# Optimization experiments

Measured on AMD Instinct MI355X. Metric: run time of the kernel, lower is better.

## Reference

```python
import jax, jax.numpy as jnp
import numpy as np

K = 9
VOCAB = 7
DIM = 512
LOW = 256  # downsampled bottleneck dim
N_LAYERS = 2
EPS = 1e-5


def _inorm(x, g, b):
    # InstanceNorm1d over length axis (biased var), x: (N, C, K)
    m = jnp.mean(x, axis=-1, keepdims=True)
    v = jnp.mean((x - m) ** 2, axis=-1, keepdims=True)
    return g[None, :, None] * (x - m) * jax.lax.rsqrt(v + EPS) + b[None, :, None]


def _conv5_same(x, w, b):
    # x: (N, C, K), w: (O, C, 5), dilation 1, padding 'same' -> pad 2
    y = jax.lax.conv_general_dilated(
        x, w, window_strides=(1,), padding=[(2, 2)],
        dimension_numbers=('NCH', 'OIH', 'NCH'))
    return y + b[None, :, None]


def _bytenet_layer(x, p):
    (g1, b1, g2, b2, g3, b3, w1, c1b, w2, c2b, w3, c3b) = p
    h = jax.nn.gelu(_inorm(x, g1, b1), approximate=False)
    h = jnp.einsum('nck,oc->nok', h, w1) + c1b[None, :, None]      # 1x1 conv 512->256
    h = jax.nn.gelu(_inorm(h, g2, b2), approximate=False)
    h = _conv5_same(h, w2, c2b)                                     # k=5 conv 256->256
    h = jax.nn.gelu(_inorm(h, g3, b3), approximate=False)
    h = jnp.einsum('nck,oc->nok', h, w3) + c3b[None, :, None]      # 1x1 conv 256->512
    return h + x  # dropout is identity in eval


def setup_inputs() -> dict:
    key = jax.random.key(0)
    ks = jax.random.split(key, 16)
    x = jax.random.randint(ks[0], (8, 2048), 0, VOCAB)
    emb = jax.random.normal(ks[1], (VOCAB, DIM), jnp.float32) * 0.02
    emb = emb.at[6].set(0.0)  # padding_idx=6
    d = {
        'x': x,
        'emb': emb,
        'ln1_w': jnp.ones((N_LAYERS, DIM)), 'ln1_b': jnp.zeros((N_LAYERS, DIM)),
        'ln2_w': jnp.ones((N_LAYERS, LOW)), 'ln2_b': jnp.zeros((N_LAYERS, LOW)),
        'ln3_w': jnp.ones((N_LAYERS, LOW)), 'ln3_b': jnp.zeros((N_LAYERS, LOW)),
        'c1_w': jax.random.normal(ks[2], (N_LAYERS, LOW, DIM), jnp.float32) * 0.02,
        'c1_b': jnp.zeros((N_LAYERS, LOW)),
        'c2_w': jax.random.normal(ks[3], (N_LAYERS, LOW, LOW, 5), jnp.float32) * 0.02,
        'c2_b': jnp.zeros((N_LAYERS, LOW)),
        'c3_w': jax.random.normal(ks[4], (N_LAYERS, DIM, LOW), jnp.float32) * 0.02,
        'c3_b': jnp.zeros((N_LAYERS, DIM)),
        'out_w': jax.random.normal(ks[5], (VOCAB, DIM * K), jnp.float32) * 0.02,
        'out_b': jnp.zeros((VOCAB,)),
    }
    return d


def reference(x, emb, ln1_w, ln1_b, ln2_w, ln2_b, ln3_w, ln3_b,
              c1_w, c1_b, c2_w, c2_b, c3_w, c3_b, out_w, out_b):
    B, L = x.shape
    W = L - K + 1
    e = emb[x]                                        # (B, L, D)
    idx = jnp.arange(W)[:, None] + jnp.arange(K)      # (W, K)
    win = e[:, idx, :]                                # (B, W, K, D)
    h = win.transpose(0, 1, 3, 2).reshape(B * W, DIM, K)  # (N, D, K)
    for i in range(N_LAYERS):
        p = (ln1_w[i], ln1_b[i], ln2_w[i], ln2_b[i], ln3_w[i], ln3_b[i],
             c1_w[i], c1_b[i], c2_w[i], c2_b[i], c3_w[i], c3_b[i])
        h = _bytenet_layer(h, p)
    pred = h.reshape(B * W, DIM * K) @ out_w.T + out_b
    return pred.reshape(B, W, VOCAB)
```

## Files before the change

### kernel.cpp

```cpp
#include <hip/hip_runtime.h>

typedef __attribute__((ext_vector_type(8))) short bfv8;
typedef __attribute__((ext_vector_type(4))) float f32x4;
typedef __attribute__((ext_vector_type(4))) unsigned short usv4;

typedef __attribute__((address_space(1))) const void gvoid;
typedef __attribute__((address_space(3))) void lvoid;
__device__ __forceinline__ void gload16(const void* g, void* l) {
  __builtin_amdgcn_global_load_lds((gvoid*)g, (lvoid*)l, 16, 0, 0);
}

__device__ __forceinline__ float bf2f(unsigned short u) {
  union { unsigned int i; float f; } c; c.i = ((unsigned int)u) << 16; return c.f;
}
__device__ __forceinline__ unsigned short f2bf(float f) {
  union { float f; unsigned int i; } c; c.f = f;
  unsigned int r = c.i + 0x7FFFu + ((c.i >> 16) & 1u);
  return (unsigned short)(r >> 16);
}
__device__ __forceinline__ float gelu_(float x) {
  float z2 = 1.5957691216057308f * x * __builtin_fmaf(0.044715f, x * x, 1.0f);
  float e = __expf(z2);
  float t = __builtin_amdgcn_rcpf(e + 1.0f);
  return x - x * t;
}
__device__ __forceinline__ int div9(int col) {
  return (int)(__umulhi((unsigned)col, 954437177u) >> 1);
}

#define CHP 132

__global__ void k_prep(const float* c1w, const float* c2w, const float* c3w,
                       const float* outw, unsigned short* W1b, unsigned short* W2t,
                       unsigned short* W3b, float* OWt) {
  int i = blockIdx.x * 256 + threadIdx.x;
  if (i < 262144) { W1b[i] = f2bf(c1w[i]); return; }
  i -= 262144;
  if (i < 655360) {
    int ii = i & 255, o = (i >> 8) & 255, rest = i >> 16;
    int t = rest % 5, l = rest / 5;
    W2t[i] = f2bf(c2w[(((l * 256 + o) << 8) + ii) * 5 + t]);
    return;
  }
  i -= 655360;
  if (i < 262144) { W3b[i] = f2bf(c3w[i]); return; }
  i -= 262144;
  if (i < 32256) {
    int c = i & 511, rk = i >> 9;
    int r = rk / 9, k = rk - 9 * r;
    OWt[i] = outw[r * 4608 + c * 9 + k];
  }
}

__global__ void k_x0(const int* x, const float* emb, unsigned short* X, int n0) {
  int idx = blockIdx.x * 256 + threadIdx.x;
  int c = idx & 511, nl = idx >> 9;
  int gn = n0 + nl, b = gn >> 11, w = gn & 2047;
  unsigned short* dst = X + (size_t)(12 + nl * 12) * 512 + c;
  for (int k = 0; k < 9; k++) {
    int t = w + k; if (t > 2047) t = 2047;
    dst[k * 512] = f2bf(emb[x[(b << 11) + t] * 512 + c]);
  }
}

__global__ void k_zpad(unsigned short* AL) {
  int i = threadIdx.x;
  for (; i < 12 * 256; i += 256) AL[i] = 0;
}

template <int MODE>
__global__ __launch_bounds__(512, 4) void k_gemm(
    const unsigned short* __restrict__ Aw, const unsigned short* __restrict__ Bsrc,
    const float* __restrict__ cbias, const float* __restrict__ n1w,
    const float* __restrict__ n1b, const float* __restrict__ gw,
    const float* __restrict__ gb, unsigned short* __restrict__ Out, int nkc) {
  __shared__ __align__(16) char smem[43008];
  unsigned short* lA = (unsigned short*)smem;
  unsigned short* lB = (unsigned short*)(smem + 32768);
  unsigned short* sE = (unsigned short*)smem;

  const int KROW = (MODE == 0) ? 512 : 256;
  int tid = threadIdx.x, wv = tid >> 6, ln = tid & 63;
  int lr = ln >> 3, lu = ln & 7;
  int m0 = (MODE == 2) ? (blockIdx.y << 8) : 0;
  int w0 = blockIdx.x << 3;
  int col0 = blockIdx.x * 72;

  int cl0 = (wv << 3) + lr;
  int colg0 = col0 + cl0; if (colg0 >= nkc) colg0 = nkc - 1;
  int brow0 = colg0 + 3 * div9(colg0) + 12;
  int bsw0 = (lu ^ (cl0 & 7)) << 3;
  int cl1 = 64 + (wv << 3) + lr;
  int colg1 = col0 + cl1; if (colg1 >= nkc) colg1 = nkc - 1;
  int brow1 = colg1 + 3 * div9(colg1) + 12;
  int bsw1 = (lu ^ (cl1 & 7)) << 3;
  int arow = (wv << 3) + lr;

  f32x4 acc[2][5];
  #pragma unroll
  for (int i = 0; i < 2; i++)
    #pragma unroll
    for (int j = 0; j < 5; j++) acc[i][j] = (f32x4){0.f, 0.f, 0.f, 0.f};

  int ksteps = (MODE == 1) ? 20 : (KROW >> 6);
  for (int ks = 0; ks < ksteps; ks++) {
    int kb, dlt; const unsigned short* Ab;
    if (MODE == 1) {
      int t = ks >> 2; kb = (ks & 3) << 6; dlt = t - 2; Ab = Aw + t * 65536;
    } else { kb = ks << 6; dlt = 0; Ab = Aw; }

    #pragma unroll
    for (int p = 0; p < 4; p++) {
      int m = (p << 6) + arow;
      gload16(Ab + (size_t)(m0 + m) * KROW + kb + ((lu ^ (m & 7)) << 3),
              lA + ((p << 6) + (wv << 3)) * 64);
    }
    gload16(Bsrc + (size_t)(brow0 + dlt) * KROW + kb + bsw0,
            lB + ((wv << 3)) * 64);
    if (wv < 2)
      gload16(Bsrc + (size_t)(brow1 + dlt) * KROW + kb + bsw1,
              lB + ((64 + (wv << 3))) * 64);
    __syncthreads();

    if (MODE == 0) {
      int gch = kb + ln;
      float gg = n1w[gch], bo = n1b[gch];
      float v[9], s = 0.f;
      #pragma unroll
      for (int k = 0; k < 9; k++) {
        int cl = wv * 9 + k;
        v[k] = bf2f(lB[cl * 64 + (((ln >> 3) ^ (cl & 7)) << 3) + (ln & 7)]);
        s += v[k];
      }
      float mn = s * (1.0f / 9.0f), q = 0.f;
      #pragma unroll
      for (int k = 0; k < 9; k++) { float d = v[k] - mn; q += d * d; }
      float r = rsqrtf(q * (1.0f / 9.0f) + 1e-5f);
      #pragma unroll
      for (int k = 0; k < 9; k++) {
        int cl = wv * 9 + k;
        lB[cl * 64 + (((ln >> 3) ^ (cl & 7)) << 3) + (ln & 7)] =
            f2bf(gelu_(gg * (v[k] - mn) * r + bo));
      }
      __syncthreads();
    }

    int l16 = ln & 15, loct = ln >> 4;
    #pragma unroll
    for (int kk = 0; kk < 2; kk++) {
      int kbyte = (kk << 6) + (loct << 4);
      bfv8 af[2], bf_[5];
      #pragma unroll
      for (int mi = 0; mi < 2; mi++) {
        int row = (wv << 5) + (mi << 4) + l16;
        af[mi] = *(const bfv8*)((const char*)lA + row * 128 + (kbyte ^ ((row & 7) << 4)));
      }
      #pragma unroll
      for (int ni = 0; ni < 5; ni++) {
        int row = (ni << 4) + l16;
        bf_[ni] = *(const bfv8*)((const char*)lB + row * 128 + (kbyte ^ ((row & 7) << 4)));
      }
      #pragma unroll
      for (int mi = 0; mi < 2; mi++)
        #pragma unroll
        for (int ni = 0; ni < 5; ni++)
          acc[mi][ni] = __builtin_amdgcn_mfma_f32_16x16x32_bf16(
              af[mi], bf_[ni], acc[mi][ni], 0, 0, 0);
    }
    __syncthreads();
  }

  int l16 = ln & 15, loct = ln >> 4;
  int c4 = tid & 31, win = tid >> 5;
  #pragma unroll
  for (int R = 0; R < 2; R++) {
    if (R) __syncthreads();
    if ((wv >> 2) == R) {
      #pragma unroll
      for (int mi = 0; mi < 2; mi++) {
        int chh = ((wv & 3) << 5) + (mi << 4) + (loct << 2);
        #pragma unroll
        for (int ni = 0; ni < 5; ni++) {
          int col = (ni << 4) + l16;
          usv4 pk;
          #pragma unroll
          for (int q = 0; q < 4; q++) pk[q] = f2bf(acc[mi][ni][q]);
          *(usv4*)(sE + col * CHP + chh) = pk;
        }
      }
    }
    __syncthreads();
    if (tid < 256) {
      int chl = (R << 7) + (c4 << 2);
      const unsigned short* sb = sE + (win * 9) * CHP + (c4 << 2);
      if (MODE == 2) {
        int chg = m0 + chl;
        size_t ob = (size_t)(12 + (size_t)(w0 + win) * 12) * 512 + chg;
        float cb[4];
        #pragma unroll
        for (int j = 0; j < 4; j++) cb[j] = cbias[chg + j];
        #pragma unroll
        for (int k = 0; k < 9; k++) {
          usv4 rv = *(const usv4*)(sb + k * CHP);
          usv4 old = *(usv4*)(Out + ob + k * 512);
          usv4 pk;
          #pragma unroll
          for (int j = 0; j < 4; j++)
            pk[j] = f2bf(bf2f(rv[j]) + cb[j] + bf2f(old[j]));
          *(usv4*)(Out + ob + k * 512) = pk;
        }
      } else {
        size_t ob = (size_t)(12 + (size_t)(w0 + win) * 12) * 256 + chl;
        float s1[4] = {0.f, 0.f, 0.f, 0.f}, s2[4] = {0.f, 0.f, 0.f, 0.f};
        #pragma unroll
        for (int k = 0; k < 9; k++) {
          usv4 rv = *(const usv4*)(sb + k * CHP);
          #pragma unroll
          for (int j = 0; j < 4; j++) {
            float f = bf2f(rv[j]);
            s1[j] += f; s2[j] = __builtin_fmaf(f, f, s2[j]);
          }
        }
        float mn[4], rr[4], gg[4], bo[4];
        #pragma unroll
        for (int j = 0; j < 4; j++) {
          mn[j] = s1[j] * (1.0f / 9.0f);
          float var = s2[j] * (1.0f / 9.0f) - mn[j] * mn[j];
          rr[j] = rsqrtf(var + 1e-5f);
          gg[j] = gw[chl + j]; bo[j] = gb[chl + j];
        }
        #pragma unroll
        for (int k = 0; k < 9; k++) {
          usv4 rv = *(const usv4*)(sb + k * CHP);
          usv4 pk;
          #pragma unroll
          for (int j = 0; j < 4; j++)
            pk[j] = f2bf(gelu_(gg[j] * (bf2f(rv[j]) - mn[j]) * rr[j] + bo[j]));
          *(usv4*)(Out + ob + k * 256) = pk;
        }
        if (MODE == 0) {
          usv4 z = (usv4){0, 0, 0, 0};
          *(usv4*)(Out + ob + 9 * 256) = z;
          *(usv4*)(Out + ob + 10 * 256) = z;
          *(usv4*)(Out + ob + 11 * 256) = z;
        }
      }
    }
  }
}

__global__ void k_out(const unsigned short* X, const float* OWt, const float* outb,
                      float* pred, int n0, int nc) {
  int gw = (blockIdx.x * 256 + threadIdx.x) >> 6;
  int ln = threadIdx.x & 63;
  if (gw >= nc) return;
  int gn = n0 + gw, b = gn >> 11, w = gn & 2047;
  if (w >= 2040) return;
  const unsigned short* xb = X + (size_t)(12 + gw * 12) * 512 + ln * 8;
  float a[7];
  #pragma unroll
  for (int r = 0; r < 7; r++) a[r] = 0.f;
  for (int k = 0; k < 9; k++) {
    bfv8 xv = *(const bfv8*)(xb + k * 512);
    float xf[8];
    #pragma unroll
    for (int j = 0; j < 8; j++) xf[j] = bf2f((unsigned short)xv[j]);
    #pragma unroll
    for (int r = 0; r < 7; r++) {
      const float* wp = OWt + (r * 9 + k) * 512 + ln * 8;
      float4 w0 = *(const float4*)(wp);
      float4 w1 = *(const float4*)(wp + 4);
      a[r] += xf[0] * w0.x + xf[1] * w0.y + xf[2] * w0.z + xf[3] * w0.w +
              xf[4] * w1.x + xf[5] * w1.y + xf[6] * w1.z + xf[7] * w1.w;
    }
  }
  #pragma unroll
  for (int r = 0; r < 7; r++)
    for (int off = 32; off; off >>= 1) a[r] += __shfl_down(a[r], off);
  if (ln == 0) {
    float* o = pred + (size_t)(b * 2040 + w) * 7;
    #pragma unroll
    for (int r = 0; r < 7; r++) o[r] = a[r] + outb[r];
  }
}

extern "C" void kernel_launch(void* const* d_in, const int* in_sizes, int n_in,
                              void* d_out, int out_size, void* d_ws, size_t ws_size,
                              hipStream_t stream) {
  const int*   x    = (const int*)d_in[0];
  const float* emb  = (const float*)d_in[1];
  const float* ln1w = (const float*)d_in[2];
  const float* ln1b = (const float*)d_in[3];
  const float* ln2w = (const float*)d_in[4];
  const float* ln2b = (const float*)d_in[5];
  const float* ln3w = (const float*)d_in[6];
  const float* ln3b = (const float*)d_in[7];
  const float* c1w  = (const float*)d_in[8];
  const float* c2w  = (const float*)d_in[10];
  const float* c3w  = (const float*)d_in[12];
  const float* c3b  = (const float*)d_in[13];
  const float* outw = (const float*)d_in[14];
  const float* outb = (const float*)d_in[15];
  float* pred = (float*)d_out;

  int nc = 16384;
  while (nc > 128 &&
         2488320ull + (unsigned long long)(nc + 1) * 24576ull > ws_size)
    nc >>= 1;
  int nkc = nc * 9;
  int tiles = nc >> 3;
  int nchunks = 16384 / nc;

  char* ws = (char*)d_ws;
  unsigned short* W1b = (unsigned short*)(ws);
  unsigned short* W2t = (unsigned short*)(ws + 524288);
  unsigned short* W3b = (unsigned short*)(ws + 1835008);
  float*          OWt = (float*)(ws + 2359296);
  char* act = ws + 2488320;
  size_t hiB = (size_t)(nc + 1) * 12288;
  size_t loB = (size_t)(nc + 1) * 6144;
  unsigned short* X   = (unsigned short*)(act);
  unsigned short* AL  = (unsigned short*)(act + hiB);
  unsigned short* AL2 = (unsigned short*)(act + hiB + loB);

  k_prep<<<(1211904 + 255) / 256, 256, 0, stream>>>(c1w, c2w, c3w, outw,
                                                    W1b, W2t, W3b, OWt);
  k_zpad<<<1, 256, 0, stream>>>(AL);

  for (int ch = 0; ch < nchunks; ch++) {
    int n0 = ch * nc;
    k_x0<<<nc * 2, 256, 0, stream>>>(x, emb, X, n0);
    for (int l = 0; l < 2; l++) {
      k_gemm<0><<<dim3(tiles, 1), 512, 0, stream>>>(
          W1b + l * 131072, X, nullptr, ln1w + l * 512, ln1b + l * 512,
          ln2w + l * 256, ln2b + l * 256, AL, nkc);
      k_gemm<1><<<dim3(tiles, 1), 512, 0, stream>>>(
          W2t + l * 327680, AL, nullptr, nullptr, nullptr,
          ln3w + l * 256, ln3b + l * 256, AL2, nkc);
      k_gemm<2><<<dim3(tiles, 2), 512, 0, stream>>>(
          W3b + l * 131072, AL2, c3b + l * 512, nullptr, nullptr,
          nullptr, nullptr, X, nkc);
    }
    k_out<<<nc / 4, 256, 0, stream>>>(X, OWt, outb, pred, n0, nc);
  }
}
```

Baseline: 844.4 us.

## Halve GEMM block to 256 threads with four M-fragments per wave

The fused GEMM kernels now run 4 waves per block instead of 8. Each wave computes a 64x80 tile (4x5 MFMA accumulators) instead of 32x80, and the A/B global-to-LDS loads, the instance-norm prologue and the epilogue are redistributed across the fewer threads. The aim is to raise the MFMA-to-LDS-read ratio per wave and cut barrier cost. In exchange it doubles accumulator registers and lowers the launch-bounds occupancy target, which could limit latency hiding.

```diff
diff --git a/kernel.cpp b/kernel.cpp
--- a/kernel.cpp
+++ b/kernel.cpp
@@ -69,7 +69,7 @@
 }
 
 template <int MODE>
-__global__ __launch_bounds__(512, 4) void k_gemm(
+__global__ __launch_bounds__(256, 3) void k_gemm(
     const unsigned short* __restrict__ Aw, const unsigned short* __restrict__ Bsrc,
     const float* __restrict__ cbias, const float* __restrict__ n1w,
     const float* __restrict__ n1b, const float* __restrict__ gw,
@@ -86,19 +86,19 @@
   int w0 = blockIdx.x << 3;
   int col0 = blockIdx.x * 72;
 
-  int cl0 = (wv << 3) + lr;
-  int colg0 = col0 + cl0; if (colg0 >= nkc) colg0 = nkc - 1;
-  int brow0 = colg0 + 3 * div9(colg0) + 12;
-  int bsw0 = (lu ^ (cl0 & 7)) << 3;
-  int cl1 = 64 + (wv << 3) + lr;
-  int colg1 = col0 + cl1; if (colg1 >= nkc) colg1 = nkc - 1;
-  int brow1 = colg1 + 3 * div9(colg1) + 12;
-  int bsw1 = (lu ^ (cl1 & 7)) << 3;
+  int brow[3], bsw[3];
+  #pragma unroll
+  for (int s = 0; s < 3; s++) {
+    int cl = (s << 5) + (wv << 3) + lr;
+    int colg = col0 + cl; if (colg >= nkc) colg = nkc - 1;
+    brow[s] = colg + 3 * div9(colg) + 12;
+    bsw[s] = (lu ^ (cl & 7)) << 3;
+  }
   int arow = (wv << 3) + lr;
 
-  f32x4 acc[2][5];
-  #pragma unroll
-  for (int i = 0; i < 2; i++)
+  f32x4 acc[4][5];
+  #pragma unroll
+  for (int i = 0; i < 4; i++)
     #pragma unroll
     for (int j = 0; j < 5; j++) acc[i][j] = (f32x4){0.f, 0.f, 0.f, 0.f};
 
@@ -110,37 +110,42 @@
     } else { kb = ks << 6; dlt = 0; Ab = Aw; }
 
     #pragma unroll
-    for (int p = 0; p < 4; p++) {
-      int m = (p << 6) + arow;
+    for (int p = 0; p < 8; p++) {
+      int m = (p << 5) + arow;
       gload16(Ab + (size_t)(m0 + m) * KROW + kb + ((lu ^ (m & 7)) << 3),
-              lA + ((p << 6) + (wv << 3)) * 64);
-    }
-    gload16(Bsrc + (size_t)(brow0 + dlt) * KROW + kb + bsw0,
-            lB + ((wv << 3)) * 64);
+              lA + ((p << 5) + (wv << 3)) * 64);
+    }
+    #pragma unroll
+    for (int s = 0; s < 2; s++)
+      gload16(Bsrc + (size_t)(brow[s] + dlt) * KROW + kb + bsw[s],
+              lB + ((s << 5) + (wv << 3)) * 64);
     if (wv < 2)
-      gload16(Bsrc + (size_t)(brow1 + dlt) * KROW + kb + bsw1,
-              lB + ((64 + (wv << 3))) * 64);
+      gload16(Bsrc + (size_t)(brow[2] + dlt) * KROW + kb + bsw[2],
+              lB + (64 + (wv << 3)) * 64);
     __syncthreads();
 
     if (MODE == 0) {
       int gch = kb + ln;
       float gg = n1w[gch], bo = n1b[gch];
-      float v[9], s = 0.f;
-      #pragma unroll
-      for (int k = 0; k < 9; k++) {
-        int cl = wv * 9 + k;
-        v[k] = bf2f(lB[cl * 64 + (((ln >> 3) ^ (cl & 7)) << 3) + (ln & 7)]);
-        s += v[k];
-      }
-      float mn = s * (1.0f / 9.0f), q = 0.f;
-      #pragma unroll
-      for (int k = 0; k < 9; k++) { float d = v[k] - mn; q += d * d; }
-      float r = rsqrtf(q * (1.0f / 9.0f) + 1e-5f);
-      #pragma unroll
-      for (int k = 0; k < 9; k++) {
-        int cl = wv * 9 + k;
-        lB[cl * 64 + (((ln >> 3) ^ (cl & 7)) << 3) + (ln & 7)] =
-            f2bf(gelu_(gg * (v[k] - mn) * r + bo));
+      #pragma unroll
+      for (int g = 0; g < 2; g++) {
+        float v[9], s = 0.f;
+        #pragma unroll
+        for (int k = 0; k < 9; k++) {
+          int cl = wv * 18 + g * 9 + k;
+          v[k] = bf2f(lB[cl * 64 + ((lr ^ (cl & 7)) << 3) + lu]);
+          s += v[k];
+        }
+        float mn = s * (1.0f / 9.0f), q = 0.f;
+        #pragma unroll
+        for (int k = 0; k < 9; k++) { float d = v[k] - mn; q += d * d; }
+        float r = rsqrtf(q * (1.0f / 9.0f) + 1e-5f);
+        #pragma unroll
+        for (int k = 0; k < 9; k++) {
+          int cl = wv * 18 + g * 9 + k;
+          lB[cl * 64 + ((lr ^ (cl & 7)) << 3) + lu] =
+              f2bf(gelu_(gg * (v[k] - mn) * r + bo));
+        }
       }
       __syncthreads();
     }
@@ -149,10 +154,10 @@
     #pragma unroll
     for (int kk = 0; kk < 2; kk++) {
       int kbyte = (kk << 6) + (loct << 4);
-      bfv8 af[2], bf_[5];
-      #pragma unroll
-      for (int mi = 0; mi < 2; mi++) {
-        int row = (wv << 5) + (mi << 4) + l16;
+      bfv8 af[4], bf_[5];
+      #pragma unroll
+      for (int mi = 0; mi < 4; mi++) {
+        int row = (wv << 6) + (mi << 4) + l16;
         af[mi] = *(const bfv8*)((const char*)lA + row * 128 + (kbyte ^ ((row & 7) << 4)));
       }
       #pragma unroll
@@ -161,7 +166,7 @@
         bf_[ni] = *(const bfv8*)((const char*)lB + row * 128 + (kbyte ^ ((row & 7) << 4)));
       }
       #pragma unroll
-      for (int mi = 0; mi < 2; mi++)
+      for (int mi = 0; mi < 4; mi++)
         #pragma unroll
         for (int ni = 0; ni < 5; ni++)
           acc[mi][ni] = __builtin_amdgcn_mfma_f32_16x16x32_bf16(
@@ -175,10 +180,10 @@
   #pragma unroll
   for (int R = 0; R < 2; R++) {
     if (R) __syncthreads();
-    if ((wv >> 2) == R) {
-      #pragma unroll
-      for (int mi = 0; mi < 2; mi++) {
-        int chh = ((wv & 3) << 5) + (mi << 4) + (loct << 2);
+    if ((wv >> 1) == R) {
+      #pragma unroll
+      for (int mi = 0; mi < 4; mi++) {
+        int chh = ((wv & 1) << 6) + (mi << 4) + (loct << 2);
         #pragma unroll
         for (int ni = 0; ni < 5; ni++) {
           int col = (ni << 4) + l16;
@@ -190,7 +195,7 @@
       }
     }
     __syncthreads();
-    if (tid < 256) {
+    {
       int chl = (R << 7) + (c4 << 2);
       const unsigned short* sb = sE + (win * 9) * CHP + (c4 << 2);
       if (MODE == 2) {
@@ -331,13 +336,13 @@
     int n0 = ch * nc;
     k_x0<<<nc * 2, 256, 0, stream>>>(x, emb, X, n0);
     for (int l = 0; l < 2; l++) {
-      k_gemm<0><<<dim3(tiles, 1), 512, 0, stream>>>(
+      k_gemm<0><<<dim3(tiles, 1), 256, 0, stream>>>(
           W1b + l * 131072, X, nullptr, ln1w + l * 512, ln1b + l * 512,
           ln2w + l * 256, ln2b + l * 256, AL, nkc);
-      k_gemm<1><<<dim3(tiles, 1), 512, 0, stream>>>(
+      k_gemm<1><<<dim3(tiles, 1), 256, 0, stream>>>(
           W2t + l * 327680, AL, nullptr, nullptr, nullptr,
           ln3w + l * 256, ln3b + l * 256, AL2, nkc);
-      k_gemm<2><<<dim3(tiles, 2), 512, 0, stream>>>(
+      k_gemm<2><<<dim3(tiles, 2), 256, 0, stream>>>(
           W3b + l * 131072, AL2, c3b + l * 512, nullptr, nullptr,
           nullptr, nullptr, X, nkc);
     }
```

Measured after the change: 907.7 us. +7.5%, slower.
